# Kernel tuning notes

Measured on AMD Instinct MI355X. Metric: run time of the kernel, lower is better.

## Reference

```python
import jax, jax.numpy as jnp
import numpy as np

N, D, K, H, G = 200000, 256, 128, 4, 1024  # nodes, emb_dim, hidden, heads, graphs


def setup_inputs() -> dict:
    key = jax.random.key(0)
    k0, k1, k2, k3 = jax.random.split(key, 4)
    node_features = jax.random.normal(k0, (N, D), jnp.float32)
    segment_ids = jnp.sort(jax.random.randint(k1, (N,), 0, G)).astype(jnp.int32)
    W1 = jax.random.normal(k2, (H, D, K), jnp.float32) / np.float32(np.sqrt(D))
    b1 = jnp.zeros((H, K), jnp.float32)
    W2 = jax.random.normal(k3, (H, K), jnp.float32) / np.float32(np.sqrt(K))
    b2 = jnp.zeros((H,), jnp.float32)
    return {"node_features": node_features, "segment_ids": segment_ids,
            "num_graphs": G, "W1": W1, "b1": b1, "W2": W2, "b2": b2}


def _segment_softmax(scores, seg, num_segments):
    # scores: [N, H]; numerically-stable softmax within each graph segment, per head
    m = jax.ops.segment_max(scores, seg, num_segments=num_segments)  # [G, H]
    e = jnp.exp(scores - m[seg])
    s = jax.ops.segment_sum(e, seg, num_segments=num_segments)  # [G, H]
    return e / s[seg]


def reference(node_features, segment_ids, num_graphs, W1, b1, W2, b2):
    # Per-head MLP score for all heads at once: [N, H]
    h = jax.nn.relu(jnp.einsum('nd,hdk->nhk', node_features, W1) + b1)
    scores = jnp.einsum('nhk,hk->nh', h, W2) + b2
    # dgl.softmax_nodes per head == segment softmax over graph ids
    attn = _segment_softmax(scores, segment_ids, num_graphs)  # [N, H]
    # combine_type == 'mean': mean_h segment_sum(attn_h * x)
    # == segment_sum(mean_h(attn_h) * x) since the sum is linear in attn.
    avg_attn = attn.mean(axis=1)  # [N]
    weighted = avg_attn[:, None] * node_features  # [N, D]
    return jax.ops.segment_sum(weighted, segment_ids, num_segments=num_graphs)  # [G, D]
```

## Files before the change

### kernel.cpp

```cpp
#include <hip/hip_runtime.h>
#include <hip/hip_bf16.h>

typedef unsigned short u16;
typedef __attribute__((ext_vector_type(8))) __bf16 bf16x8;
typedef __attribute__((ext_vector_type(8))) u16 u16x8;
typedef __attribute__((ext_vector_type(4))) float f32x4;

__device__ __forceinline__ u16 f2bf(float f) {
    unsigned u = __float_as_uint(f);
    u += 0x7fffu + ((u >> 16) & 1u);
    return (u16)(u >> 16);
}

__global__ __launch_bounds__(256) void transpose_w1(const float* __restrict__ W1,
                                                    u16* __restrict__ W1T) {
    __shared__ u16 tile[64][132];
    const int t = threadIdx.x;
    const int h = blockIdx.x >> 2;
    const int dt = blockIdx.x & 3;
#pragma unroll
    for (int j = 0; j < 8; ++j) {
        int idx = j * 256 + t;
        int r = idx >> 5;
        int kq = idx & 31;
        float4 v = *reinterpret_cast<const float4*>(
            W1 + ((size_t)h * 256 + dt * 64 + r) * 128 + kq * 4);
        ushort4 o;
        o.x = f2bf(v.x); o.y = f2bf(v.y); o.z = f2bf(v.z); o.w = f2bf(v.w);
        *reinterpret_cast<ushort4*>(&tile[r][kq * 4]) = o;
    }
    __syncthreads();
#pragma unroll
    for (int j = 0; j < 4; ++j) {
        int idx = j * 256 + t;
        int k = idx >> 3;
        int c8 = idx & 7;
        u16x8 o;
#pragma unroll
        for (int e = 0; e < 8; ++e) o[e] = tile[c8 * 8 + e][k];
        *reinterpret_cast<u16x8*>(W1T + ((size_t)h * 128 + k) * 256 + dt * 64 + c8 * 8) = o;
    }
}

__global__ __launch_bounds__(256, 2) void score_kernel(
        const float* __restrict__ x, const u16* __restrict__ W1T,
        const float* __restrict__ b1, const float* __restrict__ W2,
        const float* __restrict__ b2, float* __restrict__ scores, int N) {
    __shared__ u16 xb[16384];

    const int t = threadIdx.x;
    const int wave = t >> 6;
    const int lane = t & 63;
    const int l15 = lane & 15;
    const int quad = lane >> 4;
    const int n0 = blockIdx.x * 64;

    const u16* aptr = W1T + ((size_t)wave * 128 + l15) * 256 + quad * 8;

    bf16x8 a0[8], a1[8];
#pragma unroll
    for (int j = 0; j < 8; ++j)
        a0[j] = *reinterpret_cast<const bf16x8*>(aptr + j * 4096);

    {
        const int nrow = wave * 16 + (lane >> 2);
        const int koff = (lane & 3) * 8;
        int nn = n0 + nrow; if (nn >= N) nn = N - 1;
        const float* src = x + (size_t)nn * 256 + koff;
        const int l_t = ((lane & 3) << 4) | (lane >> 2);
        const int q   = l_t ^ ((l_t >> 4) << 1);
        u16* dst = xb + (size_t)wave * 512 + q * 8;
        float4 v[16];
#pragma unroll
        for (int i = 0; i < 8; ++i) {
            v[2 * i]     = *reinterpret_cast<const float4*>(src + i * 32);
            v[2 * i + 1] = *reinterpret_cast<const float4*>(src + i * 32 + 4);
        }
#pragma unroll
        for (int i = 0; i < 8; ++i) {
            u16x8 o;
            o[0] = f2bf(v[2*i].x);   o[1] = f2bf(v[2*i].y);
            o[2] = f2bf(v[2*i].z);   o[3] = f2bf(v[2*i].w);
            o[4] = f2bf(v[2*i+1].x); o[5] = f2bf(v[2*i+1].y);
            o[6] = f2bf(v[2*i+1].z); o[7] = f2bf(v[2*i+1].w);
            *reinterpret_cast<u16x8*>(dst + i * 2048) = o;
        }
    }

    const int qr = lane ^ ((lane >> 4) << 1);
    const u16* xrd = xb + qr * 8;

    __syncthreads();

    f32x4 acc[8][4] = {};
#pragma unroll
    for (int ks = 0; ks < 8; ++ks) {
        auto& a  = (ks & 1) ? a1 : a0;
        auto& an = (ks & 1) ? a0 : a1;
        bf16x8 b[4];
#pragma unroll
        for (int nf = 0; nf < 4; ++nf)
            b[nf] = *reinterpret_cast<const bf16x8*>(xrd + (ks * 4 + nf) * 512);
        if (ks < 7) {
#pragma unroll
            for (int j = 0; j < 8; ++j)
                an[j] = *reinterpret_cast<const bf16x8*>(aptr + j * 4096 + (ks + 1) * 32);
        }
#pragma unroll
        for (int fr = 0; fr < 8; ++fr)
#pragma unroll
            for (int nf = 0; nf < 4; ++nf)
                acc[fr][nf] = __builtin_amdgcn_mfma_f32_16x16x32_bf16(
                    a[fr], b[nf], acc[fr][nf], 0, 0, 0);
    }

    const int h = wave;
    float4 b1v[8], w2v[8];
#pragma unroll
    for (int fr = 0; fr < 8; ++fr) {
        int rb = h * 128 + fr * 16 + quad * 4;
        b1v[fr] = *reinterpret_cast<const float4*>(b1 + rb);
        w2v[fr] = *reinterpret_cast<const float4*>(W2 + rb);
    }
    const float b2v = b2[h];
#pragma unroll
    for (int nf = 0; nf < 4; ++nf) {
        float p = 0.f;
#pragma unroll
        for (int fr = 0; fr < 8; ++fr) {
            f32x4 c = acc[fr][nf];
            p += fmaxf(c[0] + b1v[fr].x, 0.f) * w2v[fr].x
               + fmaxf(c[1] + b1v[fr].y, 0.f) * w2v[fr].y
               + fmaxf(c[2] + b1v[fr].z, 0.f) * w2v[fr].z
               + fmaxf(c[3] + b1v[fr].w, 0.f) * w2v[fr].w;
        }
        p += __shfl_xor(p, 16, 64);
        p += __shfl_xor(p, 32, 64);
        int n = n0 + nf * 16 + lane;
        if (lane < 16 && n < N)
            scores[(size_t)n * 4 + h] = p + b2v;
    }
}

__device__ __forceinline__ int lower_bound(const int* __restrict__ a, int n, int v) {
    int lo = 0, hi = n;
    while (lo < hi) {
        int mid = (lo + hi) >> 1;
        if (a[mid] < v) lo = mid + 1; else hi = mid;
    }
    return lo;
}

__global__ __launch_bounds__(256) void segstat_kernel(
        const float4* __restrict__ scores4, const int* __restrict__ seg,
        float4* __restrict__ mOut, float4* __restrict__ isOut, int N) {
    __shared__ float4 redm[4];
    __shared__ float4 reds[4];
    const int g = blockIdx.x;
    const int t = threadIdx.x;
    const int start = lower_bound(seg, N, g);
    const int end = lower_bound(seg, N, g + 1);

    float4 mx = make_float4(-3.4e38f, -3.4e38f, -3.4e38f, -3.4e38f);
    for (int i = start + t; i < end; i += 256) {
        float4 s = scores4[i];
        mx.x = fmaxf(mx.x, s.x); mx.y = fmaxf(mx.y, s.y);
        mx.z = fmaxf(mx.z, s.z); mx.w = fmaxf(mx.w, s.w);
    }
#pragma unroll
    for (int off = 1; off < 64; off <<= 1) {
        mx.x = fmaxf(mx.x, __shfl_xor(mx.x, off, 64));
        mx.y = fmaxf(mx.y, __shfl_xor(mx.y, off, 64));
        mx.z = fmaxf(mx.z, __shfl_xor(mx.z, off, 64));
        mx.w = fmaxf(mx.w, __shfl_xor(mx.w, off, 64));
    }
    if ((t & 63) == 0) redm[t >> 6] = mx;
    __syncthreads();
    mx = redm[0];
#pragma unroll
    for (int w = 1; w < 4; ++w) {
        mx.x = fmaxf(mx.x, redm[w].x); mx.y = fmaxf(mx.y, redm[w].y);
        mx.z = fmaxf(mx.z, redm[w].z); mx.w = fmaxf(mx.w, redm[w].w);
    }

    float4 sm = make_float4(0.f, 0.f, 0.f, 0.f);
    for (int i = start + t; i < end; i += 256) {
        float4 s = scores4[i];
        sm.x += expf(s.x - mx.x); sm.y += expf(s.y - mx.y);
        sm.z += expf(s.z - mx.z); sm.w += expf(s.w - mx.w);
    }
#pragma unroll
    for (int off = 1; off < 64; off <<= 1) {
        sm.x += __shfl_xor(sm.x, off, 64);
        sm.y += __shfl_xor(sm.y, off, 64);
        sm.z += __shfl_xor(sm.z, off, 64);
        sm.w += __shfl_xor(sm.w, off, 64);
    }
    if ((t & 63) == 0) reds[t >> 6] = sm;
    __syncthreads();
    if (t == 0) {
        float4 tot = reds[0];
        for (int w = 1; w < 4; ++w) {
            tot.x += reds[w].x; tot.y += reds[w].y;
            tot.z += reds[w].z; tot.w += reds[w].w;
        }
        bool nonempty = end > start;
        float4 m_out = nonempty ? mx : make_float4(0.f, 0.f, 0.f, 0.f);
        float4 is;
        is.x = (nonempty && tot.x > 0.f) ? 1.f / tot.x : 0.f;
        is.y = (nonempty && tot.y > 0.f) ? 1.f / tot.y : 0.f;
        is.z = (nonempty && tot.z > 0.f) ? 1.f / tot.z : 0.f;
        is.w = (nonempty && tot.w > 0.f) ? 1.f / tot.w : 0.f;
        mOut[g] = m_out;
        isOut[g] = is;
    }
}

__global__ __launch_bounds__(256) void wsum_kernel(
        const float* __restrict__ x, const float4* __restrict__ scores4,
        const int* __restrict__ seg, const float4* __restrict__ mArr,
        const float4* __restrict__ isArr, float* __restrict__ out, int N) {
    __shared__ float wl[64];
    __shared__ int gl[64];
    __shared__ unsigned long long bmask_s;
    const int t = threadIdx.x;
    const int n0 = blockIdx.x * 64;
    const int cnt = min(64, N - n0);

    if (t < 64) {
        int g = -1;
        float w = 0.f;
        bool bnd = false;
        if (t < cnt) {
            int n = n0 + t;
            g = seg[n];
            float4 s = scores4[n];
            float4 m = mArr[g];
            float4 is = isArr[g];
            w = 0.25f * (expf(s.x - m.x) * is.x + expf(s.y - m.y) * is.y +
                         expf(s.z - m.z) * is.z + expf(s.w - m.w) * is.w);
            bnd = (t > 0) && (g != seg[n - 1]);
        }
        wl[t] = w;
        gl[t] = g;
        unsigned long long bm = __ballot(bnd);
        if (t == 0) bmask_s = bm;
    }
    __syncthreads();
    const unsigned long long bmask = bmask_s;

    int rs = 0;
    while (rs < cnt) {
        unsigned long long mm = (rs < 63) ? (bmask & ((~0ULL) << (rs + 1))) : 0ULL;
        int re = mm ? (__ffsll((long long)mm) - 1) : cnt;
        if (re > cnt) re = cnt;
        float acc = 0.f;
        int i = rs;
        for (; i + 8 <= re; i += 8) {
            float xv[8];
#pragma unroll
            for (int j = 0; j < 8; ++j)
                xv[j] = x[(size_t)(n0 + i + j) * 256 + t];
#pragma unroll
            for (int j = 0; j < 8; ++j) acc += wl[i + j] * xv[j];
        }
        for (; i < re; ++i) acc += wl[i] * x[(size_t)(n0 + i) * 256 + t];
        atomicAdd(&out[(size_t)gl[rs] * 256 + t], acc);
        rs = re;
    }
}

extern "C" void kernel_launch(void* const* d_in, const int* in_sizes, int n_in,
                              void* d_out, int out_size, void* d_ws, size_t ws_size,
                              hipStream_t stream) {
    const float* x  = (const float*)d_in[0];
    const int* seg  = (const int*)d_in[1];
    const float* W1 = (const float*)d_in[3];
    const float* b1 = (const float*)d_in[4];
    const float* W2 = (const float*)d_in[5];
    const float* b2 = (const float*)d_in[6];
    float* out = (float*)d_out;

    const int N = in_sizes[0] / 256;
    const int G = 1024;

    char* ws = (char*)d_ws;
    float* scores = (float*)ws;
    u16* W1T      = (u16*)(ws + (size_t)N * 16);
    float* mArr   = (float*)(ws + (size_t)N * 16 + 262144);
    float* isArr  = mArr + (size_t)G * 4;

    hipMemsetAsync(d_out, 0, (size_t)G * 256 * sizeof(float), stream);
    transpose_w1<<<16, 256, 0, stream>>>(W1, W1T);
    score_kernel<<<(N + 63) / 64, 256, 0, stream>>>(x, W1T, b1, W2, b2, scores, N);
    segstat_kernel<<<G, 256, 0, stream>>>((const float4*)scores, seg,
                                          (float4*)mArr, (float4*)isArr, N);
    wsum_kernel<<<(N + 63) / 64, 256, 0, stream>>>(x, (const float4*)scores, seg,
                                                   (const float4*)mArr,
                                                   (const float4*)isArr, out, N);
}
```

Before: 436.5 us.

## Stream W1 tiles via global_load_lds triple buffer instead of register double buffer

Replaces the register double-buffered global loads of the W1 fragments with direct global-to-LDS async loads into a three-stage shared-memory ring, using explicit vmcnt waits to keep two stages in flight. Each wave then reads its A fragments from LDS. This is meant to cut VGPR pressure and hide W1 load latency behind the MFMAs. It also drops launch bounds to one block per CU because LDS grows by 96KB, which reduces occupancy and latency hiding across blocks. The waits cover only the issuing wave's own loads, and since each wave reads back only its own slice of LDS, no barrier is needed.

```diff
diff --git a/kernel.cpp b/kernel.cpp
--- a/kernel.cpp
+++ b/kernel.cpp
@@ -10,6 +10,12 @@
     unsigned u = __float_as_uint(f);
     u += 0x7fffu + ((u >> 16) & 1u);
     return (u16)(u >> 16);
+}
+
+__device__ __forceinline__ void gl_lds16(const void* g, void* l) {
+    __builtin_amdgcn_global_load_lds(
+        (const __attribute__((address_space(1))) void*)g,
+        (__attribute__((address_space(3))) void*)l, 16, 0, 0);
 }
 
 __global__ __launch_bounds__(256) void transpose_w1(const float* __restrict__ W1,
@@ -42,11 +48,12 @@
     }
 }
 
-__global__ __launch_bounds__(256, 2) void score_kernel(
+__global__ __launch_bounds__(256, 1) void score_kernel(
         const float* __restrict__ x, const u16* __restrict__ W1T,
         const float* __restrict__ b1, const float* __restrict__ W2,
         const float* __restrict__ b2, float* __restrict__ scores, int N) {
     __shared__ u16 xb[16384];
+    __shared__ u16 sA[3][16384];
 
     const int t = threadIdx.x;
     const int wave = t >> 6;
@@ -55,12 +62,7 @@
     const int quad = lane >> 4;
     const int n0 = blockIdx.x * 64;
 
-    const u16* aptr = W1T + ((size_t)wave * 128 + l15) * 256 + quad * 8;
-
-    bf16x8 a0[8], a1[8];
-#pragma unroll
-    for (int j = 0; j < 8; ++j)
-        a0[j] = *reinterpret_cast<const bf16x8*>(aptr + j * 4096);
+    const u16* asrc = W1T + ((size_t)wave * 128 + l15) * 256 + quad * 8;
 
     {
         const int nrow = wave * 16 + (lane >> 2);
@@ -92,20 +94,36 @@
 
     __syncthreads();
 
+#pragma unroll
+    for (int j = 0; j < 8; ++j)
+        gl_lds16(asrc + j * 4096, &sA[0][(wave * 8 + j) * 512]);
+#pragma unroll
+    for (int j = 0; j < 8; ++j)
+        gl_lds16(asrc + j * 4096 + 32, &sA[1][(wave * 8 + j) * 512]);
+
     f32x4 acc[8][4] = {};
 #pragma unroll
     for (int ks = 0; ks < 8; ++ks) {
-        auto& a  = (ks & 1) ? a1 : a0;
-        auto& an = (ks & 1) ? a0 : a1;
-        bf16x8 b[4];
+        if (ks < 6) {
+            const int buf = (ks + 2) % 3;
+#pragma unroll
+            for (int j = 0; j < 8; ++j)
+                gl_lds16(asrc + j * 4096 + (ks + 2) * 32,
+                         &sA[buf][(wave * 8 + j) * 512]);
+        }
+        if (ks < 6)      asm volatile("s_waitcnt vmcnt(16)" ::: "memory");
+        else if (ks == 6) asm volatile("s_waitcnt vmcnt(8)" ::: "memory");
+        else              asm volatile("s_waitcnt vmcnt(0)" ::: "memory");
+        __builtin_amdgcn_sched_barrier(0);
+
+        bf16x8 a[8], b[4];
+        const u16* abase = &sA[ks % 3][wave * 4096 + lane * 8];
+#pragma unroll
+        for (int j = 0; j < 8; ++j)
+            a[j] = *reinterpret_cast<const bf16x8*>(abase + j * 512);
 #pragma unroll
         for (int nf = 0; nf < 4; ++nf)
             b[nf] = *reinterpret_cast<const bf16x8*>(xrd + (ks * 4 + nf) * 512);
-        if (ks < 7) {
-#pragma unroll
-            for (int j = 0; j < 8; ++j)
-                an[j] = *reinterpret_cast<const bf16x8*>(aptr + j * 4096 + (ks + 1) * 32);
-        }
 #pragma unroll
         for (int fr = 0; fr < 8; ++fr)
 #pragma unroll
```

After: 435.1 us. Within noise of the previous version (-0.3%).
